# Performance work log

Measured on AMD Instinct MI355X. Metric: run time of the kernel, lower is better.

## Reference

```python
import jax, jax.numpy as jnp
import numpy as np

N, F, C1, H, C2, E = 50000, 256, 32, 8, 16, 800000
NEG_SLOPE = 0.2


def gat_layer(x, src, dst, W, a_src, a_dst, b, heads, out_c, concat):
    n = x.shape[0]
    h = (x @ W).reshape(n, heads, out_c)               # [N,H,C]
    al_src = jnp.sum(h * a_src, axis=-1)               # [N,H]
    al_dst = jnp.sum(h * a_dst, axis=-1)               # [N,H]
    e = jax.nn.leaky_relu(al_src[src] + al_dst[dst], NEG_SLOPE)  # [E,H]
    # segment softmax over incoming edges of each dst node
    m = jax.ops.segment_max(e, dst, num_segments=n)
    e = jnp.exp(e - m[dst])
    denom = jax.ops.segment_sum(e, dst, num_segments=n)
    alpha = e / (denom[dst] + 1e-16)                   # [E,H]
    msg = h[src] * alpha[..., None]                    # [E,H,C]
    out = jax.ops.segment_sum(msg, dst, num_segments=n)
    out = out.reshape(n, heads * out_c) if concat else out.mean(axis=1)
    return out + b


def conv1d(x, w, b):
    # x: [1,C,N], w: [O,I,K], 'same' padding (K=5 -> pad 2)
    pad = (w.shape[-1] - 1) // 2
    y = jax.lax.conv_general_dilated(x, w, (1,), [(pad, pad)],
                                     dimension_numbers=('NCH', 'OIH', 'NCH'))
    return y + b[None, :, None]


def setup_inputs() -> dict:
    key = jax.random.key(0)
    ks = jax.random.split(key, 20)
    s = lambda k, shp, sc: jax.random.normal(k, shp, jnp.float32) * sc
    inp = {
        'x': jax.random.normal(ks[0], (N, F), jnp.float32),
        'edge_index': jax.random.randint(ks[1], (2, E), 0, N, jnp.int32),
        'W1': s(ks[2], (F, H * C1), 0.06),
        'a_src1': s(ks[3], (H, C1), 0.1), 'a_dst1': s(ks[4], (H, C1), 0.1),
        'b1': jnp.zeros((H * C1,), jnp.float32),
        'W2': s(ks[5], (H * C1, C2), 0.06),
        'a_src2': s(ks[6], (1, C2), 0.1), 'a_dst2': s(ks[7], (1, C2), 0.1),
        'b2': jnp.zeros((C2,), jnp.float32),
        'proj_w': s(ks[8], (C2, 1), 0.2), 'proj_b': jnp.zeros((1,), jnp.float32),
        'c1_w': s(ks[9], (C2, C2, 5), 0.1), 'c1_b': jnp.zeros((C2,), jnp.float32),
        'c2_w': s(ks[10], (C2, C2, 5), 0.1), 'c2_b': jnp.zeros((C2,), jnp.float32),
        'lin_w': s(ks[11], (2 * C2, C2), 0.15), 'lin_b': jnp.zeros((C2,), jnp.float32),
    }
    return inp


def reference(x, edge_index, W1, a_src1, a_dst1, b1, W2, a_src2, a_dst2, b2,
              proj_w, proj_b, c1_w, c1_b, c2_w, c2_b, lin_w, lin_b):
    n = x.shape[0]
    loops = jnp.arange(n, dtype=edge_index.dtype)
    src = jnp.concatenate([edge_index[0], loops])  # PyG GATConv adds self-loops
    dst = jnp.concatenate([edge_index[1], loops])

    h = jax.nn.relu(gat_layer(x, src, dst, W1, a_src1, a_dst1, b1, H, C1, True))
    x1 = gat_layer(h, src, dst, W2, a_src2, a_dst2, b2, 1, C2, False)  # [N,C2]

    g = (x1 @ proj_w + proj_b)[:, 0]                  # [N]
    sort_idx = jnp.argsort(g)
    inverse_idx = jnp.argsort(sort_idx)
    sorted_x = g[sort_idx][:, None] * x1[sort_idx]    # [N,C2]
    sx = sorted_x.T[None]                             # [1,C2,N]
    sx = jax.nn.relu(conv1d(sx, c1_w, c1_b))
    sx = conv1d(sx, c2_w, c2_b)
    x2 = sx[0].T[inverse_idx]                         # [N,C2]

    out = jnp.concatenate([x1, x2], axis=1) @ lin_w + lin_b
    return jax.nn.log_softmax(out, axis=1)
```

## Files before the change

kernel.cpp:

```cpp
#include <hip/hip_runtime.h>
#include <math.h>

#define NBUCKET 65536

__device__ __forceinline__ float leakyrelu02(float v) { return v > 0.f ? v : 0.2f * v; }

__global__ __launch_bounds__(256) void k_gemm1(const float* __restrict__ A,
                                               const float* __restrict__ B,
                                               float* __restrict__ C, int M) {
  __shared__ float As[16][68];
  __shared__ float Bs[16][64];
  const int m0 = blockIdx.x * 64;
  const int n0 = blockIdx.y * 64;
  const int tid = threadIdx.x;
  const int tm = tid & 15, tn = tid >> 4;
  float acc[4][4];
#pragma unroll
  for (int i = 0; i < 4; ++i)
#pragma unroll
    for (int j = 0; j < 4; ++j) acc[i][j] = 0.f;

  const int am = tid & 63, ak = (tid >> 6) << 2;
  const int bk = tid >> 4, bn = (tid & 15) << 2;

  for (int k0 = 0; k0 < 256; k0 += 16) {
    float4 av = make_float4(0.f, 0.f, 0.f, 0.f);
    if (m0 + am < M) av = *(const float4*)(A + (size_t)(m0 + am) * 256 + (k0 + ak));
    As[ak + 0][am] = av.x;
    As[ak + 1][am] = av.y;
    As[ak + 2][am] = av.z;
    As[ak + 3][am] = av.w;
    float4 bv = *(const float4*)(B + (size_t)(k0 + bk) * 256 + (n0 + bn));
    *(float4*)&Bs[bk][bn] = bv;
    __syncthreads();
#pragma unroll
    for (int kk = 0; kk < 16; ++kk) {
      float a[4], b[4];
#pragma unroll
      for (int i = 0; i < 4; ++i) a[i] = As[kk][tm * 4 + i];
#pragma unroll
      for (int j = 0; j < 4; ++j) b[j] = Bs[kk][tn * 4 + j];
#pragma unroll
      for (int i = 0; i < 4; ++i)
#pragma unroll
        for (int j = 0; j < 4; ++j) acc[i][j] += a[i] * b[j];
    }
    __syncthreads();
  }
#pragma unroll
  for (int i = 0; i < 4; ++i) {
    int m = m0 + tm * 4 + i;
    if (m < M) {
      float4 o = make_float4(acc[i][0], acc[i][1], acc[i][2], acc[i][3]);
      *(float4*)(C + (size_t)m * 256 + (n0 + tn * 4)) = o;
    }
  }
}

__global__ __launch_bounds__(256) void k_al1(const float* __restrict__ h_lin,
                                             const float* __restrict__ a_src,
                                             const float* __restrict__ a_dst,
                                             float* __restrict__ als,
                                             float* __restrict__ ald, int N) {
  int gid = blockIdx.x * 256 + threadIdx.x;
  int n = gid >> 6;
  int l = threadIdx.x & 63;
  if (n >= N) return;
  float4 h4 = *(const float4*)(h_lin + (size_t)n * 256 + l * 4);
  float4 vs = *(const float4*)(a_src + l * 4);
  float4 vd = *(const float4*)(a_dst + l * 4);
  float ps = h4.x * vs.x + h4.y * vs.y + h4.z * vs.z + h4.w * vs.w;
  float pd = h4.x * vd.x + h4.y * vd.y + h4.z * vd.z + h4.w * vd.w;
  ps += __shfl_xor(ps, 1); pd += __shfl_xor(pd, 1);
  ps += __shfl_xor(ps, 2); pd += __shfl_xor(pd, 2);
  ps += __shfl_xor(ps, 4); pd += __shfl_xor(pd, 4);
  if ((l & 7) == 0) {
    als[(size_t)n * 8 + (l >> 3)] = ps;
    ald[(size_t)n * 8 + (l >> 3)] = pd;
  }
}

__global__ __launch_bounds__(256) void k_hist(const int* __restrict__ ei,
                                              int* __restrict__ counts, int E, int N) {
  int e = blockIdx.x * 256 + threadIdx.x;
  if (e >= E + N) return;
  int d = (e < E) ? ei[E + e] : (e - E);
  atomicAdd(&counts[d], 1);
}

__global__ __launch_bounds__(1024) void k_scan(const int* __restrict__ counts,
                                               int* __restrict__ offsets,
                                               int* __restrict__ cursor, int chunk) {
  __shared__ int part[1024];
  const int t = threadIdx.x;
  const int base = t * chunk;
  int ssum = 0;
  for (int i = 0; i < chunk; i += 4) {
    int4 v = *(const int4*)(counts + base + i);
    ssum += v.x + v.y + v.z + v.w;
  }
  part[t] = ssum;
  __syncthreads();
  for (int d = 1; d < 1024; d <<= 1) {
    int v = (t >= d) ? part[t - d] : 0;
    __syncthreads();
    part[t] += v;
    __syncthreads();
  }
  int run = (t == 0) ? 0 : part[t - 1];
  for (int i = 0; i < chunk; i += 4) {
    int4 v = *(const int4*)(counts + base + i);
    int4 o;
    o.x = run; run += v.x;
    o.y = run; run += v.y;
    o.z = run; run += v.z;
    o.w = run; run += v.w;
    *(int4*)(offsets + base + i) = o;
    if (cursor) *(int4*)(cursor + base + i) = o;
  }
  if (t == 1023) offsets[1024 * chunk] = run;
}

__global__ __launch_bounds__(256) void k_scatter(const int* __restrict__ ei,
                                                 int* __restrict__ cursor,
                                                 int* __restrict__ csr_src, int E, int N) {
  int e = blockIdx.x * 256 + threadIdx.x;
  if (e >= E + N) return;
  int d, s;
  if (e < E) { d = ei[E + e]; s = ei[e]; }
  else { d = e - E; s = e - E; }
  int pos = atomicAdd(&cursor[d], 1);
  csr_src[pos] = s;
}

__global__ __launch_bounds__(256) void k_gat1(
    const float* __restrict__ h_lin, const float* __restrict__ als1,
    const float* __restrict__ ald1, const float* __restrict__ b1,
    const int* __restrict__ offsets, const int* __restrict__ csr_src,
    const float* __restrict__ W2, const float* __restrict__ a_src2,
    const float* __restrict__ a_dst2, float* __restrict__ h2,
    float* __restrict__ als2, float* __restrict__ ald2, int N) {
  __shared__ float w2s[4352];
  __shared__ float rowbuf[4][256];
  for (int i = threadIdx.x; i < 4096; i += 256) w2s[(i >> 4) * 17 + (i & 15)] = W2[i];
  __syncthreads();

  const int w = threadIdx.x >> 6;
  const int l = threadIdx.x & 63;
  const int n = blockIdx.x * 4 + w;
  if (n >= N) return;

  const int off = offsets[n];
  const int deg = offsets[n + 1] - off;

  const int h3 = l >> 3;
  const float ad3 = ald1[(size_t)n * 8 + h3];
  const float* hb = h_lin + l * 4;

  float ax = 0.f, ay = 0.f, az = 0.f, aw2 = 0.f, sw = 0.f;
  int e = 0;
  for (; e + 4 <= deg; e += 4) {
    int s0 = csr_src[off + e + 0];
    int s1 = csr_src[off + e + 1];
    int s2 = csr_src[off + e + 2];
    int s3 = csr_src[off + e + 3];
    float v0 = als1[(size_t)s0 * 8 + h3];
    float v1 = als1[(size_t)s1 * 8 + h3];
    float v2 = als1[(size_t)s2 * 8 + h3];
    float v3 = als1[(size_t)s3 * 8 + h3];
    float4 r0 = *(const float4*)(hb + (size_t)s0 * 256);
    float4 r1 = *(const float4*)(hb + (size_t)s1 * 256);
    float4 r2 = *(const float4*)(hb + (size_t)s2 * 256);
    float4 r3 = *(const float4*)(hb + (size_t)s3 * 256);
    float w0 = expf(leakyrelu02(v0 + ad3));
    float w1 = expf(leakyrelu02(v1 + ad3));
    float w2v = expf(leakyrelu02(v2 + ad3));
    float w3 = expf(leakyrelu02(v3 + ad3));
    sw += (w0 + w1) + (w2v + w3);
    ax += w0 * r0.x + w1 * r1.x + w2v * r2.x + w3 * r3.x;
    ay += w0 * r0.y + w1 * r1.y + w2v * r2.y + w3 * r3.y;
    az += w0 * r0.z + w1 * r1.z + w2v * r2.z + w3 * r3.z;
    aw2 += w0 * r0.w + w1 * r1.w + w2v * r2.w + w3 * r3.w;
  }
  for (; e < deg; ++e) {
    int s = csr_src[off + e];
    float ww = expf(leakyrelu02(als1[(size_t)s * 8 + h3] + ad3));
    float4 r = *(const float4*)(hb + (size_t)s * 256);
    sw += ww;
    ax += ww * r.x; ay += ww * r.y; az += ww * r.z; aw2 += ww * r.w;
  }
  const float inv = 1.f / (sw + 1e-16f);

  float4 bb = *(const float4*)(b1 + l * 4);
  rowbuf[w][l * 4 + 0] = fmaxf(ax * inv + bb.x, 0.f);
  rowbuf[w][l * 4 + 1] = fmaxf(ay * inv + bb.y, 0.f);
  rowbuf[w][l * 4 + 2] = fmaxf(az * inv + bb.z, 0.f);
  rowbuf[w][l * 4 + 3] = fmaxf(aw2 * inv + bb.w, 0.f);
  asm volatile("s_waitcnt lgkmcnt(0)" ::: "memory");

  const int o = l & 15;
  const int grp = l >> 4;
  float a2 = 0.f;
#pragma unroll 8
  for (int t = 0; t < 64; ++t) {
    int cc = grp * 64 + ((t + grp * 8) & 63);
    a2 += rowbuf[w][cc] * w2s[cc * 17 + o];
  }
  a2 += __shfl_xor(a2, 16);
  a2 += __shfl_xor(a2, 32);

  if (l < 16) {
    h2[(size_t)n * 16 + l] = a2;
    float ps = a2 * a_src2[l];
    float pd = a2 * a_dst2[l];
    ps += __shfl_xor(ps, 1); pd += __shfl_xor(pd, 1);
    ps += __shfl_xor(ps, 2); pd += __shfl_xor(pd, 2);
    ps += __shfl_xor(ps, 4); pd += __shfl_xor(pd, 4);
    ps += __shfl_xor(ps, 8); pd += __shfl_xor(pd, 8);
    if (l == 0) { als2[n] = ps; ald2[n] = pd; }
  }
}

__global__ __launch_bounds__(256) void k_gat2(
    const float* __restrict__ h2, const float* __restrict__ als2,
    const float* __restrict__ ald2, const float* __restrict__ b2,
    const float* __restrict__ proj_w, const float* __restrict__ proj_b,
    const int* __restrict__ offsets, const int* __restrict__ csr_src,
    float* __restrict__ x1, float* __restrict__ g,
    unsigned long long* __restrict__ keys, int* __restrict__ bhist, int N) {
  const int w = threadIdx.x >> 6;
  const int l = threadIdx.x & 63;
  const int n = blockIdx.x * 4 + w;
  if (n >= N) return;
  const int off = offsets[n];
  const int deg = offsets[n + 1] - off;
  const float ad = ald2[n];
  const int slot = l >> 4;
  const int c = l & 15;

  float acc = 0.f, sw = 0.f;
  int e0 = 0;
  for (; e0 + 8 <= deg; e0 += 8) {
    int sA = csr_src[off + e0 + slot];
    int sB = csr_src[off + e0 + 4 + slot];
    float vA = als2[sA];
    float vB = als2[sB];
    float hA = h2[(size_t)sA * 16 + c];
    float hB = h2[(size_t)sB * 16 + c];
    float wA = expf(leakyrelu02(vA + ad));
    float wB = expf(leakyrelu02(vB + ad));
    sw += wA + wB;
    acc += wA * hA + wB * hB;
  }
  for (; e0 < deg; e0 += 4) {
    int e = e0 + slot;
    if (e < deg) {
      int s = csr_src[off + e];
      float v = expf(leakyrelu02(als2[s] + ad));
      sw += v;
      acc += v * h2[(size_t)s * 16 + c];
    }
  }
  acc += __shfl_xor(acc, 16); sw += __shfl_xor(sw, 16);
  acc += __shfl_xor(acc, 32); sw += __shfl_xor(sw, 32);
  float x1v = acc / (sw + 1e-16f) + b2[c];

  float pg = x1v * proj_w[c];
  pg += __shfl_xor(pg, 1);
  pg += __shfl_xor(pg, 2);
  pg += __shfl_xor(pg, 4);
  pg += __shfl_xor(pg, 8);
  if (l < 16) x1[(size_t)n * 16 + l] = x1v;
  if (l == 0) {
    float gv = pg + proj_b[0];
    g[n] = gv;
    unsigned u = __float_as_uint(gv);
    u = (u & 0x80000000u) ? ~u : (u | 0x80000000u);
    keys[n] = (((unsigned long long)u) << 32) | (unsigned)n;
    atomicAdd(&bhist[u >> 16], 1);
  }
}

__global__ __launch_bounds__(256) void k_bscatter(const unsigned long long* __restrict__ keys,
                                                  int* __restrict__ cursor,
                                                  unsigned long long* __restrict__ bkeys, int N) {
  int n = blockIdx.x * 256 + threadIdx.x;
  if (n >= N) return;
  unsigned long long k = keys[n];
  int b = (int)(k >> 48);
  int pos = atomicAdd(&cursor[b], 1);
  bkeys[pos] = k;
}

__global__ __launch_bounds__(256) void k_brank(const unsigned long long* __restrict__ bkeys,
                                               const int* __restrict__ boffs,
                                               const float* __restrict__ g,
                                               const float* __restrict__ x1,
                                               int* __restrict__ rank,
                                               float* __restrict__ sortedv, int N) {
  int pos = blockIdx.x * 256 + threadIdx.x;
  if (pos >= N) return;
  unsigned long long k = bkeys[pos];
  int b = (int)(k >> 48);
  int lo = boffs[b], hi = boffs[b + 1];
  int r = lo;
  for (int j = lo; j < hi; ++j) r += (bkeys[j] < k) ? 1 : 0;
  int idx = (int)(unsigned)(k & 0xffffffffull);
  rank[idx] = r;
  float gv = g[idx];
#pragma unroll
  for (int c = 0; c < 16; c += 4) {
    float4 v = *(const float4*)(x1 + (size_t)idx * 16 + c);
    float4 o = make_float4(gv * v.x, gv * v.y, gv * v.z, gv * v.w);
    *(float4*)(sortedv + (size_t)r * 16 + c) = o;
  }
}

__global__ __launch_bounds__(256) void k_conv(const float* __restrict__ in,
                                              const float* __restrict__ wgt,
                                              const float* __restrict__ bias,
                                              float* __restrict__ out, int N, int relu) {
  __shared__ float s[260][17];
  __shared__ float ws[1280];
  __shared__ float bs[16];
  const int p0 = blockIdx.x * 256;
  for (int i = threadIdx.x; i < 1280; i += 256) ws[i] = wgt[i];
  if (threadIdx.x < 16) bs[threadIdx.x] = bias[threadIdx.x];
  for (int idx = threadIdx.x; idx < 260 * 16; idx += 256) {
    int lp = idx >> 4, c = idx & 15;
    int gp = p0 - 2 + lp;
    s[lp][c] = (gp >= 0 && gp < N) ? in[(size_t)gp * 16 + c] : 0.f;
  }
  __syncthreads();
  const int p = p0 + threadIdx.x;
  if (p >= N) return;
  float acc[16];
#pragma unroll
  for (int o = 0; o < 16; ++o) acc[o] = bs[o];
  for (int k = 0; k < 5; ++k) {
    for (int c = 0; c < 16; ++c) {
      float xv = s[threadIdx.x + k][c];
#pragma unroll
      for (int o = 0; o < 16; ++o) acc[o] += ws[(o * 16 + c) * 5 + k] * xv;
    }
  }
#pragma unroll
  for (int o = 0; o < 16; ++o) {
    float v = acc[o];
    if (relu) v = fmaxf(v, 0.f);
    out[(size_t)p * 16 + o] = v;
  }
}

__global__ __launch_bounds__(256) void k_final(
    const float* __restrict__ x1, const float* __restrict__ c2out,
    const int* __restrict__ rank, const float* __restrict__ lin_w,
    const float* __restrict__ lin_b, float* __restrict__ out, int N) {
  __shared__ float lw[512];
  __shared__ float lb[16];
  for (int i = threadIdx.x; i < 512; i += 256) lw[i] = lin_w[i];
  if (threadIdx.x < 16) lb[threadIdx.x] = lin_b[threadIdx.x];
  __syncthreads();
  const int n = blockIdx.x * 256 + threadIdx.x;
  if (n >= N) return;
  float xa[16], xb[16];
  const int r = rank[n];
#pragma unroll
  for (int c = 0; c < 16; c += 4) {
    float4 va = *(const float4*)(x1 + (size_t)n * 16 + c);
    float4 vb = *(const float4*)(c2out + (size_t)r * 16 + c);
    xa[c] = va.x; xa[c + 1] = va.y; xa[c + 2] = va.z; xa[c + 3] = va.w;
    xb[c] = vb.x; xb[c + 1] = vb.y; xb[c + 2] = vb.z; xb[c + 3] = vb.w;
  }
  float z[16];
#pragma unroll
  for (int o = 0; o < 16; ++o) z[o] = lb[o];
#pragma unroll
  for (int c = 0; c < 16; ++c) {
    float va = xa[c], vb = xb[c];
#pragma unroll
    for (int o = 0; o < 16; ++o) z[o] += va * lw[c * 16 + o] + vb * lw[(16 + c) * 16 + o];
  }
  float m = z[0];
#pragma unroll
  for (int o = 1; o < 16; ++o) m = fmaxf(m, z[o]);
  float ssum = 0.f;
#pragma unroll
  for (int o = 0; o < 16; ++o) ssum += expf(z[o] - m);
  float lse = m + logf(ssum);
#pragma unroll
  for (int o = 0; o < 16; ++o) out[(size_t)n * 16 + o] = z[o] - lse;
}

extern "C" void kernel_launch(void* const* d_in, const int* in_sizes, int n_in,
                              void* d_out, int out_size, void* d_ws, size_t ws_size,
                              hipStream_t stream) {
  const float* x = (const float*)d_in[0];
  const int* ei = (const int*)d_in[1];
  const float* W1 = (const float*)d_in[2];
  const float* a_src1 = (const float*)d_in[3];
  const float* a_dst1 = (const float*)d_in[4];
  const float* b1 = (const float*)d_in[5];
  const float* W2 = (const float*)d_in[6];
  const float* a_src2 = (const float*)d_in[7];
  const float* a_dst2 = (const float*)d_in[8];
  const float* b2 = (const float*)d_in[9];
  const float* proj_w = (const float*)d_in[10];
  const float* proj_b = (const float*)d_in[11];
  const float* c1_w = (const float*)d_in[12];
  const float* c1_b = (const float*)d_in[13];
  const float* c2_w = (const float*)d_in[14];
  const float* c2_b = (const float*)d_in[15];
  const float* lin_w = (const float*)d_in[16];
  const float* lin_b = (const float*)d_in[17];
  float* out = (float*)d_out;

  const int N = in_sizes[0] / 256;
  const int E = in_sizes[1] / 2;
  const int Etot = E + N;

  int chunk = (N + 1023) / 1024;
  chunk = (chunk + 3) & ~3;
  const int Npad = 1024 * chunk;

  char* ws = (char*)d_ws;
  size_t off = 0;
  auto alloc = [&](size_t bytes) -> void* {
    void* p = ws + off;
    off = (off + bytes + 255) & ~(size_t)255;
    return p;
  };
  float* h_lin = (float*)alloc((size_t)N * 256 * 4);
  float* als1 = (float*)alloc((size_t)N * 8 * 4);
  float* ald1 = (float*)alloc((size_t)N * 8 * 4);
  int* counts = (int*)alloc((size_t)Npad * 4);
  int* offsets = (int*)alloc((size_t)(Npad + 1) * 4);
  int* cursor = (int*)alloc((size_t)Npad * 4);
  int* csr_src = (int*)alloc((size_t)Etot * 4);
  float* h2 = (float*)alloc((size_t)N * 16 * 4);
  float* als2 = (float*)alloc((size_t)N * 4);
  float* ald2 = (float*)alloc((size_t)N * 4);
  float* x1 = (float*)alloc((size_t)N * 16 * 4);
  float* gbuf = (float*)alloc((size_t)N * 4);
  unsigned long long* keys = (unsigned long long*)alloc((size_t)N * 8);
  int* bhist = (int*)alloc((size_t)NBUCKET * 4);
  int* boffs = (int*)alloc((size_t)(NBUCKET + 1) * 4);
  int* bcursor = (int*)alloc((size_t)NBUCKET * 4);
  unsigned long long* bkeys = (unsigned long long*)alloc((size_t)N * 8);
  int* rank = (int*)alloc((size_t)N * 4);
  float* sortedv = (float*)alloc((size_t)N * 16 * 4);
  float* c1out = (float*)alloc((size_t)N * 16 * 4);
  float* c2out = (float*)alloc((size_t)N * 16 * 4);
  if (off > ws_size) return;

  hipMemsetAsync(counts, 0, (size_t)Npad * 4, stream);
  hipMemsetAsync(bhist, 0, (size_t)NBUCKET * 4, stream);

  dim3 gg((N + 63) / 64, 4);
  k_gemm1<<<gg, 256, 0, stream>>>(x, W1, h_lin, N);
  k_al1<<<(N + 3) / 4, 256, 0, stream>>>(h_lin, a_src1, a_dst1, als1, ald1, N);
  k_hist<<<(Etot + 255) / 256, 256, 0, stream>>>(ei, counts, E, N);
  k_scan<<<1, 1024, 0, stream>>>(counts, offsets, cursor, chunk);
  k_scatter<<<(Etot + 255) / 256, 256, 0, stream>>>(ei, cursor, csr_src, E, N);
  k_gat1<<<(N + 3) / 4, 256, 0, stream>>>(h_lin, als1, ald1, b1, offsets, csr_src,
                                          W2, a_src2, a_dst2, h2, als2, ald2, N);
  k_gat2<<<(N + 3) / 4, 256, 0, stream>>>(h2, als2, ald2, b2, proj_w, proj_b,
                                          offsets, csr_src, x1, gbuf, keys, bhist, N);
  k_scan<<<1, 1024, 0, stream>>>(bhist, boffs, bcursor, NBUCKET / 1024);
  k_bscatter<<<(N + 255) / 256, 256, 0, stream>>>(keys, bcursor, bkeys, N);
  k_brank<<<(N + 255) / 256, 256, 0, stream>>>(bkeys, boffs, gbuf, x1, rank, sortedv, N);
  k_conv<<<(N + 255) / 256, 256, 0, stream>>>(sortedv, c1_w, c1_b, c1out, N, 1);
  k_conv<<<(N + 255) / 256, 256, 0, stream>>>(c1out, c2_w, c2_b, c2out, N, 0);
  k_final<<<(N + 255) / 256, 256, 0, stream>>>(x1, c2out, rank, lin_w, lin_b, out, N);
}
```

Baseline: 537.2 us.

## Sort CSR edges by source chunk and precompute edge attention weights

```diff
diff --git a/kernel.cpp b/kernel.cpp
--- a/kernel.cpp
+++ b/kernel.cpp
@@ -2,6 +2,8 @@
 #include <math.h>
 
 #define NBUCKET 65536
+#define CHUNK_SHIFT 12
+#define NCHUNK 16
 
 __device__ __forceinline__ float leakyrelu02(float v) { return v > 0.f ? v : 0.2f * v; }
 
@@ -80,12 +82,45 @@
   }
 }
 
-__global__ __launch_bounds__(256) void k_hist(const int* __restrict__ ei,
-                                              int* __restrict__ counts, int E, int N) {
+__global__ __launch_bounds__(256) void k_hist2(const int* __restrict__ ei,
+                                               int* __restrict__ counts2, int E, int N) {
   int e = blockIdx.x * 256 + threadIdx.x;
   if (e >= E + N) return;
-  int d = (e < E) ? ei[E + e] : (e - E);
-  atomicAdd(&counts[d], 1);
+  int d, s;
+  if (e < E) { d = ei[E + e]; s = ei[e]; }
+  else { d = e - E; s = d; }
+  atomicAdd(&counts2[d * NCHUNK + (s >> CHUNK_SHIFT)], 1);
+}
+
+__global__ __launch_bounds__(256) void k_fold(const int* __restrict__ counts2,
+                                              int* __restrict__ counts, int N) {
+  int d = blockIdx.x * 256 + threadIdx.x;
+  if (d >= N) return;
+  int s = 0;
+#pragma unroll
+  for (int i = 0; i < NCHUNK; i += 4) {
+    int4 v = *(const int4*)(counts2 + (size_t)d * NCHUNK + i);
+    s += v.x + v.y + v.z + v.w;
+  }
+  counts[d] = s;
+}
+
+__global__ __launch_bounds__(256) void k_expand(const int* __restrict__ offsets,
+                                                const int* __restrict__ counts2,
+                                                int* __restrict__ cursor2, int N) {
+  int d = blockIdx.x * 256 + threadIdx.x;
+  if (d >= N) return;
+  int run = offsets[d];
+#pragma unroll
+  for (int i = 0; i < NCHUNK; i += 4) {
+    int4 v = *(const int4*)(counts2 + (size_t)d * NCHUNK + i);
+    int4 o;
+    o.x = run; run += v.x;
+    o.y = run; run += v.y;
+    o.z = run; run += v.z;
+    o.w = run; run += v.w;
+    *(int4*)(cursor2 + (size_t)d * NCHUNK + i) = o;
+  }
 }
 
 __global__ __launch_bounds__(1024) void k_scan(const int* __restrict__ counts,
@@ -121,25 +156,52 @@
   if (t == 1023) offsets[1024 * chunk] = run;
 }
 
-__global__ __launch_bounds__(256) void k_scatter(const int* __restrict__ ei,
-                                                 int* __restrict__ cursor,
-                                                 int* __restrict__ csr_src, int E, int N) {
+__global__ __launch_bounds__(256) void k_scatter_ew(
+    const int* __restrict__ ei, const float* __restrict__ als1,
+    const float* __restrict__ ald1, int* __restrict__ cursor2,
+    int* __restrict__ csr_src, int* __restrict__ csr_dst,
+    float* __restrict__ ew, int E, int N) {
   int e = blockIdx.x * 256 + threadIdx.x;
   if (e >= E + N) return;
   int d, s;
   if (e < E) { d = ei[E + e]; s = ei[e]; }
-  else { d = e - E; s = e - E; }
-  int pos = atomicAdd(&cursor[d], 1);
+  else { d = e - E; s = d; }
+  int pos = atomicAdd(&cursor2[d * NCHUNK + (s >> CHUNK_SHIFT)], 1);
   csr_src[pos] = s;
+  csr_dst[pos] = d;
+  float4 as0 = *(const float4*)(als1 + (size_t)s * 8);
+  float4 as1 = *(const float4*)(als1 + (size_t)s * 8 + 4);
+  float4 ad0 = *(const float4*)(ald1 + (size_t)d * 8);
+  float4 ad1 = *(const float4*)(ald1 + (size_t)d * 8 + 4);
+  float4 w0, w1;
+  w0.x = expf(leakyrelu02(as0.x + ad0.x));
+  w0.y = expf(leakyrelu02(as0.y + ad0.y));
+  w0.z = expf(leakyrelu02(as0.z + ad0.z));
+  w0.w = expf(leakyrelu02(as0.w + ad0.w));
+  w1.x = expf(leakyrelu02(as1.x + ad1.x));
+  w1.y = expf(leakyrelu02(as1.y + ad1.y));
+  w1.z = expf(leakyrelu02(as1.z + ad1.z));
+  w1.w = expf(leakyrelu02(as1.w + ad1.w));
+  *(float4*)(ew + (size_t)pos * 8) = w0;
+  *(float4*)(ew + (size_t)pos * 8 + 4) = w1;
+}
+
+__global__ __launch_bounds__(256) void k_ew2(const int* __restrict__ csr_src,
+                                             const int* __restrict__ csr_dst,
+                                             const float* __restrict__ als2,
+                                             const float* __restrict__ ald2,
+                                             float* __restrict__ ew2, int Etot) {
+  int t = blockIdx.x * 256 + threadIdx.x;
+  if (t >= Etot) return;
+  ew2[t] = expf(leakyrelu02(als2[csr_src[t]] + ald2[csr_dst[t]]));
 }
 
 __global__ __launch_bounds__(256) void k_gat1(
-    const float* __restrict__ h_lin, const float* __restrict__ als1,
-    const float* __restrict__ ald1, const float* __restrict__ b1,
-    const int* __restrict__ offsets, const int* __restrict__ csr_src,
-    const float* __restrict__ W2, const float* __restrict__ a_src2,
-    const float* __restrict__ a_dst2, float* __restrict__ h2,
-    float* __restrict__ als2, float* __restrict__ ald2, int N) {
+    const float* __restrict__ h_lin, const float* __restrict__ ew,
+    const float* __restrict__ b1, const int* __restrict__ offsets,
+    const int* __restrict__ csr_src, const float* __restrict__ W2,
+    const float* __restrict__ a_src2, const float* __restrict__ a_dst2,
+    float* __restrict__ h2, float* __restrict__ als2, float* __restrict__ ald2, int N) {
   __shared__ float w2s[4352];
   __shared__ float rowbuf[4][256];
   for (int i = threadIdx.x; i < 4096; i += 256) w2s[(i >> 4) * 17 + (i & 15)] = W2[i];
@@ -154,28 +216,24 @@
   const int deg = offsets[n + 1] - off;
 
   const int h3 = l >> 3;
-  const float ad3 = ald1[(size_t)n * 8 + h3];
   const float* hb = h_lin + l * 4;
 
   float ax = 0.f, ay = 0.f, az = 0.f, aw2 = 0.f, sw = 0.f;
   int e = 0;
   for (; e + 4 <= deg; e += 4) {
-    int s0 = csr_src[off + e + 0];
-    int s1 = csr_src[off + e + 1];
-    int s2 = csr_src[off + e + 2];
-    int s3 = csr_src[off + e + 3];
-    float v0 = als1[(size_t)s0 * 8 + h3];
-    float v1 = als1[(size_t)s1 * 8 + h3];
-    float v2 = als1[(size_t)s2 * 8 + h3];
-    float v3 = als1[(size_t)s3 * 8 + h3];
+    int p = off + e;
+    int s0 = csr_src[p + 0];
+    int s1 = csr_src[p + 1];
+    int s2 = csr_src[p + 2];
+    int s3 = csr_src[p + 3];
+    float w0 = ew[(size_t)(p + 0) * 8 + h3];
+    float w1 = ew[(size_t)(p + 1) * 8 + h3];
+    float w2v = ew[(size_t)(p + 2) * 8 + h3];
+    float w3 = ew[(size_t)(p + 3) * 8 + h3];
     float4 r0 = *(const float4*)(hb + (size_t)s0 * 256);
     float4 r1 = *(const float4*)(hb + (size_t)s1 * 256);
     float4 r2 = *(const float4*)(hb + (size_t)s2 * 256);
     float4 r3 = *(const float4*)(hb + (size_t)s3 * 256);
-    float w0 = expf(leakyrelu02(v0 + ad3));
-    float w1 = expf(leakyrelu02(v1 + ad3));
-    float w2v = expf(leakyrelu02(v2 + ad3));
-    float w3 = expf(leakyrelu02(v3 + ad3));
     sw += (w0 + w1) + (w2v + w3);
     ax += w0 * r0.x + w1 * r1.x + w2v * r2.x + w3 * r3.x;
     ay += w0 * r0.y + w1 * r1.y + w2v * r2.y + w3 * r3.y;
@@ -183,8 +241,9 @@
     aw2 += w0 * r0.w + w1 * r1.w + w2v * r2.w + w3 * r3.w;
   }
   for (; e < deg; ++e) {
-    int s = csr_src[off + e];
-    float ww = expf(leakyrelu02(als1[(size_t)s * 8 + h3] + ad3));
+    int p = off + e;
+    int s = csr_src[p];
+    float ww = ew[(size_t)p * 8 + h3];
     float4 r = *(const float4*)(hb + (size_t)s * 256);
     sw += ww;
     ax += ww * r.x; ay += ww * r.y; az += ww * r.z; aw2 += ww * r.w;
@@ -222,41 +281,41 @@
 }
 
 __global__ __launch_bounds__(256) void k_gat2(
-    const float* __restrict__ h2, const float* __restrict__ als2,
-    const float* __restrict__ ald2, const float* __restrict__ b2,
-    const float* __restrict__ proj_w, const float* __restrict__ proj_b,
-    const int* __restrict__ offsets, const int* __restrict__ csr_src,
-    float* __restrict__ x1, float* __restrict__ g,
-    unsigned long long* __restrict__ keys, int* __restrict__ bhist, int N) {
+    const float* __restrict__ h2, const float* __restrict__ ew2,
+    const float* __restrict__ b2, const float* __restrict__ proj_w,
+    const float* __restrict__ proj_b, const int* __restrict__ offsets,
+    const int* __restrict__ csr_src, float* __restrict__ x1,
+    float* __restrict__ g, unsigned long long* __restrict__ keys,
+    int* __restrict__ bhist, int N) {
   const int w = threadIdx.x >> 6;
   const int l = threadIdx.x & 63;
   const int n = blockIdx.x * 4 + w;
   if (n >= N) return;
   const int off = offsets[n];
   const int deg = offsets[n + 1] - off;
-  const float ad = ald2[n];
   const int slot = l >> 4;
   const int c = l & 15;
 
   float acc = 0.f, sw = 0.f;
   int e0 = 0;
   for (; e0 + 8 <= deg; e0 += 8) {
-    int sA = csr_src[off + e0 + slot];
-    int sB = csr_src[off + e0 + 4 + slot];
-    float vA = als2[sA];
-    float vB = als2[sB];
+    int pA = off + e0 + slot;
+    int pB = off + e0 + 4 + slot;
+    int sA = csr_src[pA];
+    int sB = csr_src[pB];
+    float wA = ew2[pA];
+    float wB = ew2[pB];
     float hA = h2[(size_t)sA * 16 + c];
     float hB = h2[(size_t)sB * 16 + c];
-    float wA = expf(leakyrelu02(vA + ad));
-    float wB = expf(leakyrelu02(vB + ad));
     sw += wA + wB;
     acc += wA * hA + wB * hB;
   }
   for (; e0 < deg; e0 += 4) {
     int e = e0 + slot;
     if (e < deg) {
-      int s = csr_src[off + e];
-      float v = expf(leakyrelu02(als2[s] + ad));
+      int p = off + e;
+      int s = csr_src[p];
+      float v = ew2[p];
       sw += v;
       acc += v * h2[(size_t)s * 16 + c];
     }
@@ -435,8 +494,12 @@
   float* ald1 = (float*)alloc((size_t)N * 8 * 4);
   int* counts = (int*)alloc((size_t)Npad * 4);
   int* offsets = (int*)alloc((size_t)(Npad + 1) * 4);
-  int* cursor = (int*)alloc((size_t)Npad * 4);
+  int* counts2 = (int*)alloc((size_t)N * NCHUNK * 4);
+  int* cursor2 = (int*)alloc((size_t)N * NCHUNK * 4);
   int* csr_src = (int*)alloc((size_t)Etot * 4);
+  int* csr_dst = (int*)alloc((size_t)Etot * 4);
+  float* ew = (float*)alloc((size_t)Etot * 8 * 4);
+  float* ew2 = (float*)alloc((size_t)Etot * 4);
   float* h2 = (float*)alloc((size_t)N * 16 * 4);
   float* als2 = (float*)alloc((size_t)N * 4);
   float* ald2 = (float*)alloc((size_t)N * 4);
@@ -454,17 +517,22 @@
   if (off > ws_size) return;
 
   hipMemsetAsync(counts, 0, (size_t)Npad * 4, stream);
+  hipMemsetAsync(counts2, 0, (size_t)N * NCHUNK * 4, stream);
   hipMemsetAsync(bhist, 0, (size_t)NBUCKET * 4, stream);
 
   dim3 gg((N + 63) / 64, 4);
   k_gemm1<<<gg, 256, 0, stream>>>(x, W1, h_lin, N);
   k_al1<<<(N + 3) / 4, 256, 0, stream>>>(h_lin, a_src1, a_dst1, als1, ald1, N);
-  k_hist<<<(Etot + 255) / 256, 256, 0, stream>>>(ei, counts, E, N);
-  k_scan<<<1, 1024, 0, stream>>>(counts, offsets, cursor, chunk);
-  k_scatter<<<(Etot + 255) / 256, 256, 0, stream>>>(ei, cursor, csr_src, E, N);
-  k_gat1<<<(N + 3) / 4, 256, 0, stream>>>(h_lin, als1, ald1, b1, offsets, csr_src,
+  k_hist2<<<(Etot + 255) / 256, 256, 0, stream>>>(ei, counts2, E, N);
+  k_fold<<<(N + 255) / 256, 256, 0, stream>>>(counts2, counts, N);
+  k_scan<<<1, 1024, 0, stream>>>(counts, offsets, nullptr, chunk);
+  k_expand<<<(N + 255) / 256, 256, 0, stream>>>(offsets, counts2, cursor2, N);
+  k_scatter_ew<<<(Etot + 255) / 256, 256, 0, stream>>>(ei, als1, ald1, cursor2,
+                                                       csr_src, csr_dst, ew, E, N);
+  k_gat1<<<(N + 3) / 4, 256, 0, stream>>>(h_lin, ew, b1, offsets, csr_src,
                                           W2, a_src2, a_dst2, h2, als2, ald2, N);
-  k_gat2<<<(N + 3) / 4, 256, 0, stream>>>(h2, als2, ald2, b2, proj_w, proj_b,
+  k_ew2<<<(Etot + 255) / 256, 256, 0, stream>>>(csr_src, csr_dst, als2, ald2, ew2, Etot);
+  k_gat2<<<(N + 3) / 4, 256, 0, stream>>>(h2, ew2, b2, proj_w, proj_b,
                                           offsets, csr_src, x1, gbuf, keys, bhist, N);
   k_scan<<<1, 1024, 0, stream>>>(bhist, boffs, bcursor, NBUCKET / 1024);
   k_bscatter<<<(N + 255) / 256, 256, 0, stream>>>(keys, bcursor, bkeys, N);
```

New measurement: 536.4 us. No clear change (-0.2%).
